# Kernel tuning notes

Hardware: AMD Instinct MI355X
Metric: run time of the kernel (lower is better)

Reference implementation:

```python
import jax, jax.numpy as jnp
import numpy as np

MAX_BRANCHES = 4
MAX_DEPTH = 3
BEAM_WIDTH = 2
TEMPERATURE = 0.8
MIN_SCORE_DIFF = 0.1


def _gelu(x):
    return jax.nn.gelu(x, approximate=False)  # torch nn.GELU default is exact erf


def _evaluate(x, We1, be1, We2, be2, We3, be3):
    # evaluator: Linear(H,2H) -> GELU -> Linear(2H,H) -> GELU -> Linear(H,1) -> Sigmoid
    h = _gelu(x @ We1 + be1)
    h = _gelu(h @ We2 + be2)
    return jax.nn.sigmoid(h @ We3 + be3)[..., 0]


def setup_inputs() -> dict:
    key = jax.random.key(0)
    B, S, H = 8, 2048, 512
    ks = jax.random.split(key, 8)
    s1 = 1.0 / np.sqrt(H)
    s2 = 1.0 / np.sqrt(2 * H)
    f32 = jnp.float32
    return {
        "hidden_states": jax.random.normal(ks[0], (B, S, H), f32),
        "We1": (jax.random.normal(ks[1], (H, 2 * H), f32) * s1),
        "be1": jnp.zeros((2 * H,), f32),
        "We2": (jax.random.normal(ks[2], (2 * H, H), f32) * s2),
        "be2": jnp.zeros((H,), f32),
        "We3": (jax.random.normal(ks[3], (H, 1), f32) * s1),
        "be3": jnp.zeros((1,), f32),
        "Wp": (jax.random.normal(ks[4], (H, H), f32) * s1),
        "bp": jnp.zeros((H,), f32),
        "Wb": (jax.random.normal(ks[5], (MAX_BRANCHES, H, H), f32) * s1),
        "bb": jnp.zeros((MAX_BRANCHES, H), f32),
    }


def reference(hidden_states, We1, be1, We2, be2, We3, be3, Wp, bp, Wb, bb):
    B, S, H = hidden_states.shape
    ev = lambda x: _evaluate(x, We1, be1, We2, be2, We3, be3)

    x0 = jnp.swapaxes(hidden_states, 0, 1)        # [S, B, H] positions independent
    beam_states = x0[:, None]                     # [S, K=1, B, H]
    beam_scores = ev(x0).mean(-1)[:, None]        # [S, 1] root score (mean over batch)

    for _ in range(MAX_DEPTH):
        K = beam_states.shape[1]
        proj = beam_states @ Wp + bp                                  # [S,K,B,H]
        # fixed per-branch projection + GELU -> thoughts [S,K,N,B,H]
        th = _gelu(jnp.einsum('skbh,nhj->sknbj', proj, Wb)
                   + bb[None, None, :, None, :])
        sc = ev(th).mean(-1) / TEMPERATURE                            # [S,K,N]

        # min_score_diff dedup: keep branch i iff no previously-kept score within
        # MIN_SCORE_DIFF and fewer than BEAM_WIDTH kept so far (static loop over 4)
        keep = jnp.zeros(sc.shape, bool)
        count = jnp.zeros(sc.shape[:-1], sc.dtype)
        for i in range(MAX_BRANCHES):
            mind = jnp.where(keep, jnp.abs(sc[..., i:i + 1] - sc), jnp.inf).min(-1)
            ki = ((count == 0) | (mind >= MIN_SCORE_DIFF)) & (count < BEAM_WIDTH)
            keep = keep.at[..., i].set(ki)
            count = count + ki.astype(count.dtype)

        cand_sc = jnp.where(keep, sc, -jnp.inf).reshape(S, K * MAX_BRANCHES)
        cand_st = th.reshape(S, K * MAX_BRANCHES, B, H)
        top_sc, top_idx = jax.lax.top_k(cand_sc, BEAM_WIDTH)          # sorted desc
        top_st = jnp.take_along_axis(cand_st, top_idx[:, :, None, None], axis=1)
        # fewer than BEAM_WIDTH survivors -> duplicate the best (same final result)
        valid = jnp.isfinite(top_sc)
        beam_scores = jnp.where(valid, top_sc, top_sc[:, :1])
        beam_states = jnp.where(valid[:, :, None, None], top_st, top_st[:, :1])

    best = beam_states[:, 0]                      # beam sorted desc -> slot 0 is best leaf
    return jnp.swapaxes(best, 0, 1) + hidden_states
```

## Files before the change

kernel.cpp:

```cpp
#include <hip/hip_runtime.h>

#define S_  2048
#define B_  8
#define CM_ 8192
#define KS_ 16

typedef _Float16 f16x8 __attribute__((ext_vector_type(8)));
typedef float    f32x4 __attribute__((ext_vector_type(4)));

__device__ __forceinline__ float gelu_f(float x){
    return 0.5f * x * (1.0f + erff(x * 0.7071067811865476f));
}


__global__ __launch_bounds__(256)
void prep_k(const float* __restrict__ src, _Float16* __restrict__ dst,
            int K, int N)
{
    int g = blockIdx.x * 256 + threadIdx.x;
    int KS = K >> 5;
    int l  = g & 63;
    int rem = g >> 6;
    int ks = rem % KS;
    int fc = rem / KS;
    int kbase = ks * 32 + (l >> 4) * 8;
    int col   = fc * 16 + (l & 15);
    size_t KN = (size_t)K * N;
    #pragma unroll
    for (int j = 0; j < 8; j++) {
        float x = src[(size_t)(kbase + j) * N + col];
        _Float16 h1 = (_Float16)x;
        _Float16 h2 = (_Float16)((x - (float)h1) * 2048.0f);
        dst[(size_t)g * 8 + j]      = h1;
        dst[KN + (size_t)g * 8 + j] = h2;
    }
}

__global__ __launch_bounds__(256)
void prep_hidden_k(const float* __restrict__ hidden, _Float16* __restrict__ dst,
                   size_t PS)
{
    int g = blockIdx.x * 256 + threadIdx.x;
    int l  = g & 63;
    int rem = g >> 6;
    int ks = rem & 15;
    int fr = rem >> 4;
    int gr = fr * 16 + (l & 15);
    int s = gr >> 3, b = gr & 7;
    int kbase = ks * 32 + (l >> 4) * 8;
    const float* src = hidden + ((size_t)b * S_ + s) * 512 + kbase;
    #pragma unroll
    for (int j = 0; j < 8; j++) {
        float x = src[j];
        _Float16 h1 = (_Float16)x;
        _Float16 h2 = (_Float16)((x - (float)h1) * 2048.0f);
        dst[(size_t)g * 8 + j]      = h1;
        dst[PS + (size_t)g * 8 + j] = h2;
    }
}

template<bool GELU, int EPI, int AMAP, bool PRED>
__global__ __launch_bounds__(256)
void fgemm(const _Float16* __restrict__ Ap, size_t aPS,
           const _Float16* __restrict__ Bp, size_t bPS, int fc0,
           const float* __restrict__ bias,
           _Float16* __restrict__ Cp, size_t cPS,
           float* __restrict__ Cf,
           const int* __restrict__ sel, int nsel, int r0)
{
    const int t    = threadIdx.x;
    const int m0   = blockIdx.x * 64;
    const int n0   = blockIdx.y * 128;
    const int lane = t & 63;
    const int wave = t >> 6;
    const int wr   = wave >> 1;
    const int wc   = wave & 1;

    const _Float16* ap[2];
    #pragma unroll
    for (int i = 0; i < 2; i++) {
        if (AMAP == 0) {
            int tl = (m0 >> 4) + wr * 2 + i;
            ap[i] = Ap + ((size_t)tl * KS_) * 512 + lane * 8;
        } else if (AMAP == 2) {
            int s = ((r0 + m0) >> 4) + wr * 2 + i;
            int j = (lane >> 3) & 1;
            int kb = sel[s * 2 + j] >> 2;
            int al = (lane & 48) | (kb << 3) | (lane & 7);
            ap[i] = Ap + ((size_t)s * KS_) * 512 + al * 8;
        } else {
            int s = ((r0 + m0) >> 4) + wr * 2 + i;
            int ti = s >> 1;
            int al = (lane & 48) | ((s & 1) << 3) | (lane & 7);
            ap[i] = Ap + ((size_t)ti * KS_) * 512 + al * 8;
        }
    }

    const _Float16* bjp[4];
    #pragma unroll
    for (int j = 0; j < 4; j++) {
        int fcg = fc0 + (n0 >> 4) + wc * 4 + j;
        bjp[j] = Bp + (size_t)fcg * KS_ * 512 + lane * 8;
    }

    f32x4 accM[2][4], accX[2][4];
    #pragma unroll
    for (int i = 0; i < 2; i++)
        #pragma unroll
        for (int j = 0; j < 4; j++) { accM[i][j] = (f32x4)0.0f; accX[i][j] = (f32x4)0.0f; }

    #pragma unroll 2
    for (int ks = 0; ks < KS_; ks++) {
        f16x8 a1[2], a2[2], b1[4], b2[4];
        #pragma unroll
        for (int i = 0; i < 2; i++) {
            a1[i] = *(const f16x8*)(ap[i] + (size_t)ks * 512);
            a2[i] = *(const f16x8*)(ap[i] + aPS + (size_t)ks * 512);
        }
        #pragma unroll
        for (int j = 0; j < 4; j++) {
            b1[j] = *(const f16x8*)(bjp[j] + (size_t)ks * 512);
            b2[j] = *(const f16x8*)(bjp[j] + bPS + (size_t)ks * 512);
        }
        #pragma unroll
        for (int i = 0; i < 2; i++)
            #pragma unroll
            for (int j = 0; j < 4; j++)
                accM[i][j] = __builtin_amdgcn_mfma_f32_16x16x32_f16(a1[i], b1[j], accM[i][j], 0, 0, 0);
        #pragma unroll
        for (int i = 0; i < 2; i++)
            #pragma unroll
            for (int j = 0; j < 4; j++)
                accX[i][j] = __builtin_amdgcn_mfma_f32_16x16x32_f16(a1[i], b2[j], accX[i][j], 0, 0, 0);
        #pragma unroll
        for (int i = 0; i < 2; i++)
            #pragma unroll
            for (int j = 0; j < 4; j++)
                accX[i][j] = __builtin_amdgcn_mfma_f32_16x16x32_f16(a2[i], b1[j], accX[i][j], 0, 0, 0);
    }

    const float inv2048 = 4.8828125e-4f;

    if (EPI == 2 || EPI == 3) {
        #pragma unroll
        for (int j = 0; j < 4; j++) {
            int lc = wc * 64 + j * 16 + (lane & 15);
            #pragma unroll
            for (int i = 0; i < 2; i++) {
                int lr = wr * 32 + i * 16 + ((lane >> 4) << 2);
                #pragma unroll
                for (int r = 0; r < 4; r++) {
                    float c = accM[i][j][r] + accX[i][j][r] * inv2048;
                    size_t idx = (size_t)(m0 + lr + r) * 512 + n0 + lc;
                    if (EPI == 3) {
                        c += Cf[idx] + bias[n0 + lc];
                        if (GELU) c = gelu_f(c);
                    }
                    Cf[idx] = c;
                }
            }
        }
        return;
    }

    __shared__ _Float16 sH1[64][136];
    __shared__ _Float16 sH2[64][136];
    #pragma unroll
    for (int j = 0; j < 4; j++) {
        int lc = wc * 64 + j * 16 + (lane & 15);
        float bv = bias[n0 + lc];
        #pragma unroll
        for (int i = 0; i < 2; i++) {
            int lr = wr * 32 + i * 16 + ((lane >> 4) << 2);
            #pragma unroll
            for (int r = 0; r < 4; r++) {
                float c = accM[i][j][r] + accX[i][j][r] * inv2048 + bv;
                if (GELU) c = gelu_f(c);
                _Float16 h1 = (_Float16)c;
                sH1[lr + r][lc] = h1;
                sH2[lr + r][lc] = (_Float16)((c - (float)h1) * 2048.0f);
            }
        }
    }
    __syncthreads();

    bool ok = true;
    if (PRED) {
        int prow = r0 + m0 + wave * 16 + (lane & 15);
        ok = ((sel[prow >> 3] & 3) == nsel);
    }
    if (ok) {
        int row = wave * 16 + (lane & 15);
        #pragma unroll
        for (int ksx = 0; ksx < 4; ksx++) {
            int coff = ksx * 32 + ((lane >> 4) << 3);
            f16x8 h1v = *(const f16x8*)&sH1[row][coff];
            f16x8 h2v = *(const f16x8*)&sH2[row][coff];
            size_t o = (((size_t)((m0 >> 4) + wave) * KS_) + (n0 >> 5) + ksx) * 512 + lane * 8;
            *(f16x8*)(Cp + o)       = h1v;
            *(f16x8*)(Cp + cPS + o) = h2v;
        }
    }
}

__global__ __launch_bounds__(256)
void score1_k(const float* __restrict__ h2, const float* __restrict__ We3,
              const float* __restrict__ be3, float* __restrict__ ev,
              int pr0, int n)
{
    int row  = blockIdx.x * 4 + (threadIdx.x >> 6);
    int lane = threadIdx.x & 63;
    const float* p = h2 + (size_t)row * 512;
    float s = 0.f;
    #pragma unroll
    for (int j = 0; j < 8; j++) s += p[lane + 64 * j] * We3[lane + 64 * j];
    #pragma unroll
    for (int off = 32; off > 0; off >>= 1) s += __shfl_down(s, off, 64);
    if (lane == 0) {
        int pr = pr0 + row;
        ev[(size_t)(pr >> 3) * 32 + n * 8 + (pr & 7)] = 1.0f / (1.0f + expf(-(s + be3[0])));
    }
}

__global__ __launch_bounds__(256)
void score2_k(const float* __restrict__ ev, float* __restrict__ sc, int n)
{
    int i = blockIdx.x * 256 + threadIdx.x;
    if (i >= n) return;
    float s = 0.f;
    #pragma unroll
    for (int b = 0; b < 8; b++) s += ev[i * 8 + b];
    sc[i] = (s * 0.125f) / 0.8f;
}

__global__ __launch_bounds__(256)
void select_k(const float* __restrict__ sc, int* __restrict__ sel, int K)
{
    int s = blockIdx.x * 256 + threadIdx.x;
    if (s >= S_) return;
    int K4 = K * 4;
    float cand[8];
    for (int k = 0; k < K; k++) {
        const float* scp = sc + (size_t)(s * K + k) * 4;
        bool keep[4] = {false, false, false, false};
        int count = 0;
        for (int i = 0; i < 4; i++) {
            float mind = INFINITY;
            for (int j = 0; j < 4; j++)
                if (keep[j]) mind = fminf(mind, fabsf(scp[i] - scp[j]));
            bool ki = ((count == 0) || (mind >= 0.1f)) && (count < 2);
            keep[i] = ki;
            if (ki) count++;
        }
        for (int i = 0; i < 4; i++) cand[k * 4 + i] = keep[i] ? scp[i] : -INFINITY;
    }
    int i0 = 0;
    for (int i = 1; i < K4; i++) if (cand[i] > cand[i0]) i0 = i;
    int i1 = -1;
    for (int i = 0; i < K4; i++) {
        if (i == i0) continue;
        if (i1 < 0 || cand[i] > cand[i1]) i1 = i;
    }
    if (!(cand[i1] > -INFINITY)) i1 = i0;
    sel[s * 2 + 0] = i0;
    sel[s * 2 + 1] = i1;
}

__global__ __launch_bounds__(256)
void final_add_k(const _Float16* __restrict__ beamsF, size_t PS,
                 const float* __restrict__ hidden, float* __restrict__ out)
{
    int tid = blockIdx.x * 256 + threadIdx.x;
    int oc = tid & 63;
    int rem = tid >> 6;
    int b = rem & 7;
    int s = rem >> 3;
    size_t o = (((size_t)s * KS_) + (oc >> 2)) * 512 + ((((oc & 3) << 4) | b) * 8);
    f16x8 m = *(const f16x8*)(beamsF + o);
    f16x8 x = *(const f16x8*)(beamsF + PS + o);
    const float* hp = hidden + ((size_t)b * S_ + s) * 512 + oc * 8;
    float* op = out + ((size_t)b * S_ + s) * 512 + oc * 8;
    #pragma unroll
    for (int j = 0; j < 8; j++)
        op[j] = (float)m[j] + (float)x[j] * 4.8828125e-4f + hp[j];
}

extern "C" void kernel_launch(void* const* d_in, const int* in_sizes, int n_in,
                              void* d_out, int out_size, void* d_ws, size_t ws_size,
                              hipStream_t stream)
{
    const float* hidden = (const float*)d_in[0];
    const float* We1 = (const float*)d_in[1];
    const float* be1 = (const float*)d_in[2];
    const float* We2 = (const float*)d_in[3];
    const float* be2 = (const float*)d_in[4];
    const float* We3 = (const float*)d_in[5];
    const float* be3 = (const float*)d_in[6];
    const float* Wp  = (const float*)d_in[7];
    const float* bp  = (const float*)d_in[8];
    const float* Wb  = (const float*)d_in[9];
    const float* bb  = (const float*)d_in[10];
    (void)in_sizes; (void)n_in; (void)ws_size;

    _Float16* beamsF = (_Float16*)d_ws;
    const size_t PS_B = 16777216;
    _Float16* R1     = beamsF + 2 * PS_B;
    const size_t PS_C = 4194304;
    _Float16* projcF = R1;
    _Float16* thcF   = R1 + 2 * PS_C;
    _Float16* h1hF   = R1 + 4 * PS_C;
    const size_t PS_G = 8388608;
    _Float16* projgF = R1;

    float* outf = (float*)d_out;
    float* evb  = outf + (out_size - 131072);
    float* scb  = evb - 16384;
    int*   sel  = (int*)(scb - 4096);
    float* h2f  = (float*)sel - 4194304;
    _Float16* WpP  = (_Float16*)(h2f - 2359296);
    _Float16* WbP  = WpP + 524288;
    _Float16* We1P = WbP + 2097152;
    _Float16* We2Pa= We1P + 1048576;
    _Float16* We2Pb= We2Pa + 524288;

    prep_k<<<128, 256, 0, stream>>>(Wp, WpP, 512, 512);
    for (int n = 0; n < 4; n++)
        prep_k<<<128, 256, 0, stream>>>(Wb + (size_t)n * 262144, WbP + (size_t)n * 524288, 512, 512);
    prep_k<<<256, 256, 0, stream>>>(We1, We1P, 512, 1024);
    prep_k<<<128, 256, 0, stream>>>(We2, We2Pa, 512, 512);
    prep_k<<<128, 256, 0, stream>>>(We2 + 262144, We2Pb, 512, 512);
    prep_hidden_k<<<4096, 256, 0, stream>>>(hidden, beamsF, PS_B);

    dim3 g1(128, 4), g2(256, 4);

    for (int d = 0; d < 3; d++) {
        const int K  = (d == 0) ? 1 : 2;
        const int NC = (d == 0) ? 2 : 4;

        for (int c = 0; c < NC; c++) {
            size_t off = (size_t)c * CM_ * 512;
            fgemm<false, 0, 0, false><<<g1, 256, 0, stream>>>(
                beamsF + off, PS_B, WpP, 262144, 0, bp, projcF, PS_C, nullptr, nullptr, 0, 0);
            for (int n = 0; n < 4; n++) {
                fgemm<true, 0, 0, false><<<g1, 256, 0, stream>>>(
                    projcF, PS_C, WbP + (size_t)n * 524288, 262144, 0, bb + n * 512,
                    thcF, PS_C, nullptr, nullptr, 0, 0);
                for (int h = 0; h < 2; h++) {
                    fgemm<true, 0, 0, false><<<g1, 256, 0, stream>>>(
                        thcF, PS_C, We1P, 524288, h * 32, be1 + h * 512,
                        h1hF, PS_C, nullptr, nullptr, 0, 0);
                    if (h == 0)
                        fgemm<false, 2, 0, false><<<g1, 256, 0, stream>>>(
                            h1hF, PS_C, We2Pa, 262144, 0, nullptr, nullptr, 0, h2f, nullptr, 0, 0);
                    else
                        fgemm<true, 3, 0, false><<<g1, 256, 0, stream>>>(
                            h1hF, PS_C, We2Pb, 262144, 0, be2, nullptr, 0, h2f, nullptr, 0, 0);
                }
                score1_k<<<2048, 256, 0, stream>>>(h2f, We3, be3, evb, c * CM_, n);
            }
        }

        const int nsc = S_ * K * 4;
        score2_k<<<(nsc + 255) / 256, 256, 0, stream>>>(evb, scb, nsc);
        select_k<<<8, 256, 0, stream>>>(scb, sel, K);

        for (int cc = 0; cc < 2; cc++) {
            int c2 = 1 - cc;
            int r0 = c2 * 16384;
            if (d == 0)
                fgemm<false, 0, 3, false><<<g2, 256, 0, stream>>>(
                    beamsF, PS_B, WpP, 262144, 0, bp, projgF, PS_G, nullptr, sel, 0, r0);
            else
                fgemm<false, 0, 2, false><<<g2, 256, 0, stream>>>(
                    beamsF, PS_B, WpP, 262144, 0, bp, projgF, PS_G, nullptr, sel, 0, r0);
            for (int n = 0; n < 4; n++)
                fgemm<true, 0, 0, true><<<g2, 256, 0, stream>>>(
                    projgF, PS_G, WbP + (size_t)n * 524288, 262144, 0, bb + n * 512,
                    beamsF + (size_t)r0 * 512, PS_B, nullptr, sel, n, r0);
        }
    }

    final_add_k<<<4096, 256, 0, stream>>>(beamsF, PS_B, hidden, outf);
}
```

Baseline: 6.377 ms.

## Stage A tiles via async global-to-LDS loads, shrink tiles, unify evaluator GEMMs

The fp16-split GEMM now loads its A operand into double-buffered shared memory with global_load_lds, so the next k-slab is prefetched while MFMAs run. The output tile per block is halved to 64x64, with occupancy raised via launch bounds. The evaluator MLP now runs as one full-width We1 GEMM followed by one K=1024 We2 GEMM writing split-fp16 output. This replaces the two-halves scheme with its fp32 read-modify-write accumulator, and the score kernel reads that fp16 output directly. In exchange there are more blocks, each with less register reuse of B, plus extra syncthreads per k-pair and a larger h1 buffer.

```diff
diff --git a/kernel.cpp b/kernel.cpp
--- a/kernel.cpp
+++ b/kernel.cpp
@@ -3,7 +3,6 @@
 #define S_  2048
 #define B_  8
 #define CM_ 8192
-#define KS_ 16
 
 typedef _Float16 f16x8 __attribute__((ext_vector_type(8)));
 typedef float    f32x4 __attribute__((ext_vector_type(4)));
@@ -11,6 +10,10 @@
 __device__ __forceinline__ float gelu_f(float x){
     return 0.5f * x * (1.0f + erff(x * 0.7071067811865476f));
 }
+
+#define GLOAD_LDS(gp, lp) __builtin_amdgcn_global_load_lds( \
+    (const __attribute__((address_space(1))) void*)(gp), \
+    (__attribute__((address_space(3))) void*)(lp), 16, 0, 0)
 
 
 __global__ __launch_bounds__(256)
@@ -59,115 +62,116 @@
     }
 }
 
-template<bool GELU, int EPI, int AMAP, bool PRED>
-__global__ __launch_bounds__(256)
+template<bool GELU, int KSN, int CKS, int AMAP, bool PRED>
+__global__ __launch_bounds__(256, 4)
 void fgemm(const _Float16* __restrict__ Ap, size_t aPS,
-           const _Float16* __restrict__ Bp, size_t bPS, int fc0,
+           const _Float16* __restrict__ Bp, size_t bPS,
            const float* __restrict__ bias,
            _Float16* __restrict__ Cp, size_t cPS,
-           float* __restrict__ Cf,
            const int* __restrict__ sel, int nsel, int r0)
 {
+    __shared__ __align__(16) char smem[32768];
     const int t    = threadIdx.x;
     const int m0   = blockIdx.x * 64;
-    const int n0   = blockIdx.y * 128;
+    const int n0   = blockIdx.y * 64;
     const int lane = t & 63;
     const int wave = t >> 6;
     const int wr   = wave >> 1;
     const int wc   = wave & 1;
 
-    const _Float16* ap[2];
-    #pragma unroll
-    for (int i = 0; i < 2; i++) {
+    const _Float16* sap;
+    {
+        int i = wave;
         if (AMAP == 0) {
-            int tl = (m0 >> 4) + wr * 2 + i;
-            ap[i] = Ap + ((size_t)tl * KS_) * 512 + lane * 8;
+            int tl = (m0 >> 4) + i;
+            sap = Ap + ((size_t)tl * KSN) * 512 + lane * 8;
         } else if (AMAP == 2) {
-            int s = ((r0 + m0) >> 4) + wr * 2 + i;
+            int s = ((r0 + m0) >> 4) + i;
             int j = (lane >> 3) & 1;
             int kb = sel[s * 2 + j] >> 2;
             int al = (lane & 48) | (kb << 3) | (lane & 7);
-            ap[i] = Ap + ((size_t)s * KS_) * 512 + al * 8;
+            sap = Ap + ((size_t)s * KSN) * 512 + al * 8;
         } else {
-            int s = ((r0 + m0) >> 4) + wr * 2 + i;
+            int s = ((r0 + m0) >> 4) + i;
             int ti = s >> 1;
             int al = (lane & 48) | ((s & 1) << 3) | (lane & 7);
-            ap[i] = Ap + ((size_t)ti * KS_) * 512 + al * 8;
-        }
-    }
-
-    const _Float16* bjp[4];
-    #pragma unroll
-    for (int j = 0; j < 4; j++) {
-        int fcg = fc0 + (n0 >> 4) + wc * 4 + j;
-        bjp[j] = Bp + (size_t)fcg * KS_ * 512 + lane * 8;
-    }
-
-    f32x4 accM[2][4], accX[2][4];
+            sap = Ap + ((size_t)ti * KSN) * 512 + al * 8;
+        }
+    }
+
+    const _Float16* bjp[2];
+    #pragma unroll
+    for (int j = 0; j < 2; j++) {
+        int fcg = (n0 >> 4) + wc * 2 + j;
+        bjp[j] = Bp + (size_t)fcg * KSN * 512 + lane * 8;
+    }
+
+    f32x4 accM[2][2], accX[2][2];
     #pragma unroll
     for (int i = 0; i < 2; i++)
         #pragma unroll
-        for (int j = 0; j < 4; j++) { accM[i][j] = (f32x4)0.0f; accX[i][j] = (f32x4)0.0f; }
-
-    #pragma unroll 2
-    for (int ks = 0; ks < KS_; ks++) {
-        f16x8 a1[2], a2[2], b1[4], b2[4];
-        #pragma unroll
-        for (int i = 0; i < 2; i++) {
-            a1[i] = *(const f16x8*)(ap[i] + (size_t)ks * 512);
-            a2[i] = *(const f16x8*)(ap[i] + aPS + (size_t)ks * 512);
-        }
-        #pragma unroll
-        for (int j = 0; j < 4; j++) {
-            b1[j] = *(const f16x8*)(bjp[j] + (size_t)ks * 512);
-            b2[j] = *(const f16x8*)(bjp[j] + bPS + (size_t)ks * 512);
-        }
-        #pragma unroll
-        for (int i = 0; i < 2; i++)
-            #pragma unroll
-            for (int j = 0; j < 4; j++)
-                accM[i][j] = __builtin_amdgcn_mfma_f32_16x16x32_f16(a1[i], b1[j], accM[i][j], 0, 0, 0);
-        #pragma unroll
-        for (int i = 0; i < 2; i++)
-            #pragma unroll
-            for (int j = 0; j < 4; j++)
-                accX[i][j] = __builtin_amdgcn_mfma_f32_16x16x32_f16(a1[i], b2[j], accX[i][j], 0, 0, 0);
-        #pragma unroll
-        for (int i = 0; i < 2; i++)
-            #pragma unroll
-            for (int j = 0; j < 4; j++)
-                accX[i][j] = __builtin_amdgcn_mfma_f32_16x16x32_f16(a2[i], b1[j], accX[i][j], 0, 0, 0);
+        for (int j = 0; j < 2; j++) { accM[i][j] = (f32x4)0.0f; accX[i][j] = (f32x4)0.0f; }
+
+    auto stage = [&](int buf, int p) {
+        #pragma unroll
+        for (int pl = 0; pl < 2; pl++)
+            #pragma unroll
+            for (int kk = 0; kk < 2; kk++) {
+                const _Float16* g = sap + (size_t)(p * 2 + kk) * 512 + (size_t)pl * aPS;
+                char* l = smem + ((((buf * 2 + pl) * 4 + wave) * 2) + kk) * 1024;
+                GLOAD_LDS(g, l);
+            }
+    };
+
+    const int NP = KSN / 2;
+    stage(0, 0);
+    __syncthreads();
+
+    int buf = 0;
+    for (int p = 0; p < NP; p++) {
+        if (p + 1 < NP) stage(buf ^ 1, p + 1);
+        #pragma unroll
+        for (int kk = 0; kk < 2; kk++) {
+            const int ks = p * 2 + kk;
+            f16x8 b1[2], b2[2], a1[2], a2[2];
+            #pragma unroll
+            for (int j = 0; j < 2; j++) {
+                b1[j] = *(const f16x8*)(bjp[j] + (size_t)ks * 512);
+                b2[j] = *(const f16x8*)(bjp[j] + bPS + (size_t)ks * 512);
+            }
+            #pragma unroll
+            for (int i = 0; i < 2; i++) {
+                const char* l1 = smem + ((((buf * 2 + 0) * 4 + (wr * 2 + i)) * 2) + kk) * 1024 + lane * 16;
+                const char* l2 = smem + ((((buf * 2 + 1) * 4 + (wr * 2 + i)) * 2) + kk) * 1024 + lane * 16;
+                a1[i] = *(const f16x8*)l1;
+                a2[i] = *(const f16x8*)l2;
+            }
+            #pragma unroll
+            for (int i = 0; i < 2; i++)
+                #pragma unroll
+                for (int j = 0; j < 2; j++)
+                    accM[i][j] = __builtin_amdgcn_mfma_f32_16x16x32_f16(a1[i], b1[j], accM[i][j], 0, 0, 0);
+            #pragma unroll
+            for (int i = 0; i < 2; i++)
+                #pragma unroll
+                for (int j = 0; j < 2; j++)
+                    accX[i][j] = __builtin_amdgcn_mfma_f32_16x16x32_f16(a1[i], b2[j], accX[i][j], 0, 0, 0);
+            #pragma unroll
+            for (int i = 0; i < 2; i++)
+                #pragma unroll
+                for (int j = 0; j < 2; j++)
+                    accX[i][j] = __builtin_amdgcn_mfma_f32_16x16x32_f16(a2[i], b1[j], accX[i][j], 0, 0, 0);
+        }
+        __syncthreads();
+        buf ^= 1;
     }
 
     const float inv2048 = 4.8828125e-4f;
-
-    if (EPI == 2 || EPI == 3) {
-        #pragma unroll
-        for (int j = 0; j < 4; j++) {
-            int lc = wc * 64 + j * 16 + (lane & 15);
-            #pragma unroll
-            for (int i = 0; i < 2; i++) {
-                int lr = wr * 32 + i * 16 + ((lane >> 4) << 2);
-                #pragma unroll
-                for (int r = 0; r < 4; r++) {
-                    float c = accM[i][j][r] + accX[i][j][r] * inv2048;
-                    size_t idx = (size_t)(m0 + lr + r) * 512 + n0 + lc;
-                    if (EPI == 3) {
-                        c += Cf[idx] + bias[n0 + lc];
-                        if (GELU) c = gelu_f(c);
-                    }
-                    Cf[idx] = c;
-                }
-            }
-        }
-        return;
-    }
-
-    __shared__ _Float16 sH1[64][136];
-    __shared__ _Float16 sH2[64][136];
-    #pragma unroll
-    for (int j = 0; j < 4; j++) {
-        int lc = wc * 64 + j * 16 + (lane & 15);
+    _Float16 (*sH1)[72] = (_Float16 (*)[72])smem;
+    _Float16 (*sH2)[72] = (_Float16 (*)[72])(smem + 9216);
+    #pragma unroll
+    for (int j = 0; j < 2; j++) {
+        int lc = wc * 32 + j * 16 + (lane & 15);
         float bv = bias[n0 + lc];
         #pragma unroll
         for (int i = 0; i < 2; i++) {
@@ -185,18 +189,15 @@
     __syncthreads();
 
     bool ok = true;
-    if (PRED) {
-        int prow = r0 + m0 + wave * 16 + (lane & 15);
-        ok = ((sel[prow >> 3] & 3) == nsel);
-    }
+    if (PRED) ok = ((sel[(r0 + m0 + wave * 16 + (lane & 15)) >> 3] & 3) == nsel);
     if (ok) {
         int row = wave * 16 + (lane & 15);
         #pragma unroll
-        for (int ksx = 0; ksx < 4; ksx++) {
+        for (int ksx = 0; ksx < 2; ksx++) {
             int coff = ksx * 32 + ((lane >> 4) << 3);
             f16x8 h1v = *(const f16x8*)&sH1[row][coff];
             f16x8 h2v = *(const f16x8*)&sH2[row][coff];
-            size_t o = (((size_t)((m0 >> 4) + wave) * KS_) + (n0 >> 5) + ksx) * 512 + lane * 8;
+            size_t o = (((size_t)((m0 >> 4) + wave) * CKS) + (n0 >> 5) + ksx) * 512 + lane * 8;
             *(f16x8*)(Cp + o)       = h1v;
             *(f16x8*)(Cp + cPS + o) = h2v;
         }
@@ -204,16 +205,21 @@
 }
 
 __global__ __launch_bounds__(256)
-void score1_k(const float* __restrict__ h2, const float* __restrict__ We3,
-              const float* __restrict__ be3, float* __restrict__ ev,
-              int pr0, int n)
+void score1f_k(const _Float16* __restrict__ h2F, size_t PS,
+               const float* __restrict__ We3, const float* __restrict__ be3,
+               float* __restrict__ ev, int pr0, int n)
 {
     int row  = blockIdx.x * 4 + (threadIdx.x >> 6);
     int lane = threadIdx.x & 63;
-    const float* p = h2 + (size_t)row * 512;
+    int tile = row >> 4, r16 = row & 15;
+    size_t o = (((size_t)tile * 16 + (lane >> 2)) * 64 + (((lane & 3) << 4) | r16)) * 8;
+    f16x8 m = *(const f16x8*)(h2F + o);
+    f16x8 x = *(const f16x8*)(h2F + PS + o);
+    int k0 = (lane >> 2) * 32 + (lane & 3) * 8;
     float s = 0.f;
     #pragma unroll
-    for (int j = 0; j < 8; j++) s += p[lane + 64 * j] * We3[lane + 64 * j];
+    for (int j = 0; j < 8; j++)
+        s += ((float)m[j] + (float)x[j] * 4.8828125e-4f) * We3[k0 + j];
     #pragma unroll
     for (int off = 32; off > 0; off >>= 1) s += __shfl_down(s, off, 64);
     if (lane == 0) {
@@ -275,7 +281,7 @@
     int rem = tid >> 6;
     int b = rem & 7;
     int s = rem >> 3;
-    size_t o = (((size_t)s * KS_) + (oc >> 2)) * 512 + ((((oc & 3) << 4) | b) * 8);
+    size_t o = (((size_t)s * 16) + (oc >> 2)) * 512 + ((((oc & 3) << 4) | b) * 8);
     f16x8 m = *(const f16x8*)(beamsF + o);
     f16x8 x = *(const f16x8*)(beamsF + PS + o);
     const float* hp = hidden + ((size_t)b * S_ + s) * 512 + oc * 8;
@@ -306,57 +312,53 @@
     const size_t PS_B = 16777216;
     _Float16* R1     = beamsF + 2 * PS_B;
     const size_t PS_C = 4194304;
+    const size_t PS_H = 8388608;
+    const size_t PS_G = 8388608;
     _Float16* projcF = R1;
     _Float16* thcF   = R1 + 2 * PS_C;
-    _Float16* h1hF   = R1 + 4 * PS_C;
-    const size_t PS_G = 8388608;
+    _Float16* h1F    = R1 + 4 * PS_C;
     _Float16* projgF = R1;
 
     float* outf = (float*)d_out;
     float* evb  = outf + (out_size - 131072);
     float* scb  = evb - 16384;
     int*   sel  = (int*)(scb - 4096);
-    float* h2f  = (float*)sel - 4194304;
-    _Float16* WpP  = (_Float16*)(h2f - 2359296);
+    _Float16* h2F = (_Float16*)((float*)sel - 4194304);
+    _Float16* WpP  = h2F - 4718592;
     _Float16* WbP  = WpP + 524288;
     _Float16* We1P = WbP + 2097152;
-    _Float16* We2Pa= We1P + 1048576;
-    _Float16* We2Pb= We2Pa + 524288;
+    _Float16* We2P = We1P + 1048576;
 
     prep_k<<<128, 256, 0, stream>>>(Wp, WpP, 512, 512);
     for (int n = 0; n < 4; n++)
         prep_k<<<128, 256, 0, stream>>>(Wb + (size_t)n * 262144, WbP + (size_t)n * 524288, 512, 512);
     prep_k<<<256, 256, 0, stream>>>(We1, We1P, 512, 1024);
-    prep_k<<<128, 256, 0, stream>>>(We2, We2Pa, 512, 512);
-    prep_k<<<128, 256, 0, stream>>>(We2 + 262144, We2Pb, 512, 512);
+    prep_k<<<256, 256, 0, stream>>>(We2, We2P, 1024, 512);
     prep_hidden_k<<<4096, 256, 0, stream>>>(hidden, beamsF, PS_B);
 
-    dim3 g1(128, 4), g2(256, 4);
+    dim3 gP(128, 8);
+    dim3 gW1(128, 16);
+    dim3 gG(256, 8);
 
     for (int d = 0; d < 3; d++) {
         const int K  = (d == 0) ? 1 : 2;
         const int NC = (d == 0) ? 2 : 4;
 
         for (int c = 0; c < NC; c++) {
-            size_t off = (size_t)c * CM_ * 512;
-            fgemm<false, 0, 0, false><<<g1, 256, 0, stream>>>(
-                beamsF + off, PS_B, WpP, 262144, 0, bp, projcF, PS_C, nullptr, nullptr, 0, 0);
+            fgemm<false, 16, 16, 0, false><<<gP, 256, 0, stream>>>(
+                beamsF + (size_t)c * CM_ * 512, PS_B, WpP, 262144, bp,
+                projcF, PS_C, nullptr, 0, 0);
             for (int n = 0; n < 4; n++) {
-                fgemm<true, 0, 0, false><<<g1, 256, 0, stream>>>(
-                    projcF, PS_C, WbP + (size_t)n * 524288, 262144, 0, bb + n * 512,
-                    thcF, PS_C, nullptr, nullptr, 0, 0);
-                for (int h = 0; h < 2; h++) {
-                    fgemm<true, 0, 0, false><<<g1, 256, 0, stream>>>(
-                        thcF, PS_C, We1P, 524288, h * 32, be1 + h * 512,
-                        h1hF, PS_C, nullptr, nullptr, 0, 0);
-                    if (h == 0)
-                        fgemm<false, 2, 0, false><<<g1, 256, 0, stream>>>(
-                            h1hF, PS_C, We2Pa, 262144, 0, nullptr, nullptr, 0, h2f, nullptr, 0, 0);
-                    else
-                        fgemm<true, 3, 0, false><<<g1, 256, 0, stream>>>(
-                            h1hF, PS_C, We2Pb, 262144, 0, be2, nullptr, 0, h2f, nullptr, 0, 0);
-                }
-                score1_k<<<2048, 256, 0, stream>>>(h2f, We3, be3, evb, c * CM_, n);
+                fgemm<true, 16, 16, 0, false><<<gP, 256, 0, stream>>>(
+                    projcF, PS_C, WbP + (size_t)n * 524288, 262144, bb + n * 512,
+                    thcF, PS_C, nullptr, 0, 0);
+                fgemm<true, 16, 32, 0, false><<<gW1, 256, 0, stream>>>(
+                    thcF, PS_C, We1P, 524288, be1,
+                    h1F, PS_H, nullptr, 0, 0);
+                fgemm<true, 32, 16, 0, false><<<gP, 256, 0, stream>>>(
+                    h1F, PS_H, We2P, 524288, be2,
+                    h2F, PS_C, nullptr, 0, 0);
+                score1f_k<<<2048, 256, 0, stream>>>(h2F, PS_C, We3, be3, evb, c * CM_, n);
             }
         }
 
@@ -368,15 +370,15 @@
             int c2 = 1 - cc;
             int r0 = c2 * 16384;
             if (d == 0)
-                fgemm<false, 0, 3, false><<<g2, 256, 0, stream>>>(
-                    beamsF, PS_B, WpP, 262144, 0, bp, projgF, PS_G, nullptr, sel, 0, r0);
+                fgemm<false, 16, 16, 3, false><<<gG, 256, 0, stream>>>(
+                    beamsF, PS_B, WpP, 262144, bp, projgF, PS_G, sel, 0, r0);
             else
-                fgemm<false, 0, 2, false><<<g2, 256, 0, stream>>>(
-                    beamsF, PS_B, WpP, 262144, 0, bp, projgF, PS_G, nullptr, sel, 0, r0);
+                fgemm<false, 16, 16, 2, false><<<gG, 256, 0, stream>>>(
+                    beamsF, PS_B, WpP, 262144, bp, projgF, PS_G, sel, 0, r0);
             for (int n = 0; n < 4; n++)
-                fgemm<true, 0, 0, true><<<g2, 256, 0, stream>>>(
-                    projgF, PS_G, WbP + (size_t)n * 524288, 262144, 0, bb + n * 512,
-                    beamsF + (size_t)r0 * 512, PS_B, nullptr, sel, n, r0);
+                fgemm<true, 16, 16, 0, true><<<gG, 256, 0, stream>>>(
+                    projgF, PS_G, WbP + (size_t)n * 524288, 262144, bb + n * 512,
+                    beamsF + (size_t)r0 * 512, PS_B, sel, n, r0);
         }
     }
 
```

Result: faster. 5.542 ms (-13.1%).
